# Kernel optimization log

Hardware: AMD Instinct MI355X
Metric: run time of the kernel (lower is better)

The kernel has to match this reference:

```python
import jax, jax.numpy as jnp
import numpy as np

N = 50000
E = 1600000
F = 128
G = 64  # number of graphs in the batch


def gat_layer(x, src, dst, W, a_src, a_dst, bias, heads, out_dim, concat):
    n = x.shape[0]
    h = (x @ W).reshape(n, heads, out_dim)                      # [N,H,D]
    alpha_src = jnp.sum(h * a_src, axis=-1)                     # [N,H]
    alpha_dst = jnp.sum(h * a_dst, axis=-1)                     # [N,H]
    e = jax.nn.leaky_relu(alpha_src[src] + alpha_dst[dst], negative_slope=0.2)  # [E,H]
    # segment softmax over edges grouped by destination node
    m = jax.ops.segment_max(e, dst, num_segments=n)
    m = jnp.where(jnp.isfinite(m), m, 0.0)
    ex = jnp.exp(e - m[dst])
    denom = jax.ops.segment_sum(ex, dst, num_segments=n)
    alpha = ex / (denom[dst] + 1e-16)                           # [E,H]
    msg = h[src] * alpha[:, :, None]                            # [E,H,D]
    out = jax.ops.segment_sum(msg, dst, num_segments=n)         # [N,H,D]
    if concat:
        out = out.reshape(n, heads * out_dim)
    else:
        out = out.mean(axis=1)
    return out + bias


def setup_inputs() -> dict:
    key = jax.random.key(0)
    ks = jax.random.split(key, 12)
    x = jax.random.normal(ks[0], (N, F), dtype=jnp.float32)
    edge_index = jax.random.randint(ks[1], (2, E), 0, N, dtype=jnp.int32)
    batch = jnp.sort(jax.random.randint(ks[2], (N,), 0, G, dtype=jnp.int32))
    s = 0.1
    W1 = jax.random.normal(ks[3], (F, 4 * 32), dtype=jnp.float32) * s
    a_src1 = jax.random.normal(ks[4], (4, 32), dtype=jnp.float32) * s
    a_dst1 = jax.random.normal(ks[5], (4, 32), dtype=jnp.float32) * s
    b1 = jnp.zeros((4 * 32,), dtype=jnp.float32)
    W2 = jax.random.normal(ks[6], (4 * 32, 2 * 16), dtype=jnp.float32) * s
    a_src2 = jax.random.normal(ks[7], (2, 16), dtype=jnp.float32) * s
    a_dst2 = jax.random.normal(ks[8], (2, 16), dtype=jnp.float32) * s
    b2 = jnp.zeros((16,), dtype=jnp.float32)
    fcW = jax.random.normal(ks[9], (16, 1), dtype=jnp.float32) * s
    fcb = jnp.zeros((1,), dtype=jnp.float32)
    return {"x": x, "edge_index": edge_index, "batch": batch,
            "W1": W1, "a_src1": a_src1, "a_dst1": a_dst1, "b1": b1,
            "W2": W2, "a_src2": a_src2, "a_dst2": a_dst2, "b2": b2,
            "fcW": fcW, "fcb": fcb}


def reference(x, edge_index, batch, W1, a_src1, a_dst1, b1, W2, a_src2, a_dst2, b2, fcW, fcb):
    n = x.shape[0]
    # PyG GATConv default: add self loops
    loops = jnp.arange(n, dtype=edge_index.dtype)
    src = jnp.concatenate([edge_index[0], loops])
    dst = jnp.concatenate([edge_index[1], loops])
    # eval mode: dropouts are no-ops
    h = jax.nn.relu(gat_layer(x, src, dst, W1, a_src1, a_dst1, b1, 4, 32, True))
    h = gat_layer(h, src, dst, W2, a_src2, a_dst2, b2, 2, 16, False)
    # global mean pool over graphs
    sums = jax.ops.segment_sum(h, batch, num_segments=G)        # [G,16]
    counts = jax.ops.segment_sum(jnp.ones((n,), h.dtype), batch, num_segments=G)
    pooled = sums / jnp.maximum(counts, 1.0)[:, None]
    return pooled @ fcW + fcb                                   # [G,1]
```

## Files before the change

kernel.cpp:

```cpp
#include <hip/hip_runtime.h>

#define LRELU(x) ((x) > 0.f ? (x) : 0.2f*(x))
typedef unsigned int uint;

__device__ inline unsigned short f2bf(float f) {
    union { float f; unsigned u; } v; v.f = f;
    unsigned r = v.u + 0x7FFF + ((v.u >> 16) & 1);
    return (unsigned short)(r >> 16);
}
__device__ inline uint packbf(float a, float b) {
    return (uint)f2bf(a) | ((uint)f2bf(b) << 16);
}
__device__ inline float bflo(uint u){ union{uint u; float f;}v; v.u = u<<16; return v.f; }
__device__ inline float bfhi(uint u){ union{uint u; float f;}v; v.u = u & 0xFFFF0000u; return v.f; }
__device__ inline float f4get(const float4& v, int i) {
    return i==0 ? v.x : i==1 ? v.y : i==2 ? v.z : v.w;
}


#define CSR_SHIFT 7
#define CSR_NBLK  512

__global__ __launch_bounds__(256) void bucket_count_kernel(
    const int* __restrict__ dst, int E, int chunk, int nb,
    int* __restrict__ blockCntT)
{
    __shared__ int cnt[1024];
    int t = threadIdx.x, k = blockIdx.x;
    for (int i = t; i < nb; i += 256) cnt[i] = 0;
    __syncthreads();
    int e0 = k * chunk, e1 = min(e0 + chunk, E);
    for (int e = e0 + t; e < e1; e += 256)
        atomicAdd(&cnt[dst[e] >> CSR_SHIFT], 1);
    __syncthreads();
    for (int b = t; b < nb; b += 256)
        blockCntT[b * CSR_NBLK + k] = cnt[b];
}

__global__ __launch_bounds__(512) void row_scan_kernel(
    int* __restrict__ blockCntT, int* __restrict__ tot)
{
    __shared__ int sm[512];
    int b = blockIdx.x, t = threadIdx.x;
    int* row = blockCntT + b * CSR_NBLK;
    int v = row[t];
    sm[t] = v;
    __syncthreads();
    for (int off = 1; off < 512; off <<= 1) {
        int u = (t >= off) ? sm[t - off] : 0;
        __syncthreads(); sm[t] += u; __syncthreads();
    }
    row[t] = sm[t] - v;
    if (t == 511) tot[b] = sm[511];
}

__global__ __launch_bounds__(1024) void total_scan_kernel(
    const int* __restrict__ tot, int nb, int* __restrict__ bucketBase)
{
    __shared__ int sm[1024];
    int t = threadIdx.x;
    int v = (t < nb) ? tot[t] : 0;
    sm[t] = v;
    __syncthreads();
    for (int off = 1; off < 1024; off <<= 1) {
        int u = (t >= off) ? sm[t - off] : 0;
        __syncthreads(); sm[t] += u; __syncthreads();
    }
    if (t < nb) bucketBase[t] = sm[t] - v;
    if (t == 1023) bucketBase[nb] = sm[1023];
}

__global__ __launch_bounds__(256) void bucket_scatter_kernel(
    const int* __restrict__ src, const int* __restrict__ dst, int E, int chunk, int nb,
    const int* __restrict__ blockCntT, const int* __restrict__ bucketBase,
    uint* __restrict__ ebuf)
{
    __shared__ int cur[1024];
    int t = threadIdx.x, k = blockIdx.x;
    for (int b = t; b < nb; b += 256)
        cur[b] = bucketBase[b] + blockCntT[b * CSR_NBLK + k];
    __syncthreads();
    int e0 = k * chunk, e1 = min(e0 + chunk, E);
    for (int e = e0 + t; e < e1; e += 256) {
        int d = dst[e], s_ = src[e];
        int pos = atomicAdd(&cur[d >> CSR_SHIFT], 1);
        ebuf[pos] = ((uint)s_ << 7) | (uint)(d & 127);
    }
}

__global__ __launch_bounds__(256) void local_csr_kernel(
    const uint* __restrict__ ebuf, const int* __restrict__ bucketBase,
    int n, int E, int* __restrict__ rowptr, int* __restrict__ csr)
{
    __shared__ int lbase[1 << CSR_SHIFT];
    __shared__ int lcur[1 << CSR_SHIFT];
    __shared__ int ldeg[1 << CSR_SHIFT];
    int b = blockIdx.x, t = threadIdx.x;
    int n0 = b << CSR_SHIFT;
    int base = bucketBase[b], end = bucketBase[b + 1];
    if (t < (1 << CSR_SHIFT)) ldeg[t] = 0;
    __syncthreads();
    for (int e = base + t; e < end; e += 256)
        atomicAdd(&ldeg[ebuf[e] & 127], 1);
    __syncthreads();
    if (t == 0) {
        int run = base;
        for (int i = 0; i < (1 << CSR_SHIFT); ++i) {
            lbase[i] = run; lcur[i] = run; run += ldeg[i];
        }
    }
    __syncthreads();
    int node = n0 + t;
    if (t < (1 << CSR_SHIFT) && node < n) rowptr[node] = lbase[t];
    if (b == 0 && t == 0) rowptr[n] = E;
    for (int e = base + t; e < end; e += 256) {
        uint ed = ebuf[e];
        int pos = atomicAdd(&lcur[ed & 127], 1);
        csr[pos] = (int)(ed >> 7);
    }
}


template<int COLS, int HEADS>
__global__ __launch_bounds__(256) void gemm_alpha_kernel(
    const float* __restrict__ x, const float* __restrict__ W,
    const float* __restrict__ a_src, const float* __restrict__ a_dst,
    uint* __restrict__ hq, float* __restrict__ as_out,
    float* __restrict__ ad_out, int n)
{
    constexpr int K = 128;
    constexpr int CPT = COLS / 8;
    constexpr int NPT = 4;
    constexpr int DIM = COLS / HEADS;
    constexpr int TPH = DIM / CPT;
    constexpr int NSLOT = COLS / 4;
    __shared__ float4 WL[K * NSLOT];

    int t = threadIdx.x;
    for (int idx = t * 4; idx < K * COLS; idx += 1024) {
        float4 w = *(const float4*)(W + idx);
        int k = idx / COLS, c = idx % COLS;
        int slot = c >> 2;
        if (COLS == 128) slot = (slot >> 2) | ((slot & 3) << 3);
        WL[k * NSLOT + slot] = w;
    }
    __syncthreads();

    int m_ = t & 7;
    int node0 = blockIdx.x * (32 * NPT) + (t >> 3) * NPT;
    if (node0 >= n) return;
    int c0 = m_ * CPT;

    const float* xr[NPT];
#pragma unroll
    for (int i = 0; i < NPT; i++) xr[i] = x + (size_t)min(node0 + i, n - 1) * K;

    float acc[NPT][CPT];
#pragma unroll
    for (int i = 0; i < NPT; i++)
#pragma unroll
        for (int q = 0; q < CPT; q++) acc[i][q] = 0.f;

    for (int k4 = 0; k4 < K; k4 += 4) {
        float4 xv[NPT];
#pragma unroll
        for (int i = 0; i < NPT; i++) xv[i] = *(const float4*)(xr[i] + k4);
#pragma unroll
        for (int kk = 0; kk < 4; kk++) {
#pragma unroll
            for (int j = 0; j < CPT / 4; j++) {
                int slot = (COLS == 128) ? (m_ | (j << 3)) : m_;
                float4 w = WL[(k4 + kk) * NSLOT + slot];
#pragma unroll
                for (int i = 0; i < NPT; i++) {
                    float xa = f4get(xv[i], kk);
                    acc[i][j*4+0] += xa * w.x;
                    acc[i][j*4+1] += xa * w.y;
                    acc[i][j*4+2] += xa * w.z;
                    acc[i][j*4+3] += xa * w.w;
                }
            }
        }
    }

    int head = c0 / DIM, lc = c0 - head * DIM;
    float asc[CPT], adc[CPT];
#pragma unroll
    for (int q = 0; q < CPT; q++) {
        asc[q] = a_src[head * DIM + lc + q];
        adc[q] = a_dst[head * DIM + lc + q];
    }

#pragma unroll
    for (int i = 0; i < NPT; i++) {
        int node = node0 + i;
        if (node >= n) break;
        if constexpr (COLS == 128) {
            uint wds[4];
#pragma unroll
            for (int j = 0; j < 4; j++) {
                int u = 0;
                u = __builtin_amdgcn_cvt_pk_fp8_f32(acc[i][j*4+0], acc[i][j*4+1], u, false);
                u = __builtin_amdgcn_cvt_pk_fp8_f32(acc[i][j*4+2], acc[i][j*4+3], u, true);
                wds[j] = (uint)u;
            }
            *(uint4*)(hq + (size_t)node * 32 + m_ * 4) = make_uint4(wds[0], wds[1], wds[2], wds[3]);
        } else {
            uint w0 = packbf(acc[i][0], acc[i][1]);
            uint w1 = packbf(acc[i][2], acc[i][3]);
            *(uint2*)(hq + (size_t)node * 16 + m_ * 2) = make_uint2(w0, w1);
        }
        float ps = 0.f, pd = 0.f;
#pragma unroll
        for (int q = 0; q < CPT; q++) {
            ps += acc[i][q] * asc[q];
            pd += acc[i][q] * adc[q];
        }
#pragma unroll
        for (int off = 1; off < TPH; off <<= 1) {
            ps += __shfl_xor(ps, off);
            pd += __shfl_xor(pd, off);
        }
        if ((m_ & (TPH - 1)) == 0) {
            as_out[node * HEADS + head] = ps;
            ad_out[node * HEADS + head] = pd;
        }
    }
}


__global__ __launch_bounds__(256) void agg1_kernel(
    const float* __restrict__ as1f, const float* __restrict__ ad1f,
    const uint* __restrict__ h1q, const int* __restrict__ rowptr,
    const int* __restrict__ csr, const float* __restrict__ b1,
    float* __restrict__ hout, int n)
{
    int t = threadIdx.x;
    int w = t >> 6, tw = t & 63;
    int g = tw >> 3, l = tw & 7;
    int head = l >> 1;
    int node = blockIdx.x * 4 + w;
    if (node >= n) return;

    float adh = ad1f[node * 4 + head];
    int rp = rowptr[node], re = rowptr[node + 1];

    float acc[16];
#pragma unroll
    for (int i = 0; i < 16; i++) acc[i] = 0.f;
    float den = 0.f;

#pragma unroll 2
    for (int e = rp + g; e < re; e += 8) {
        int s = csr[e];
        float a = as1f[s * 4 + head];
        uint4 u = *(const uint4*)(h1q + ((size_t)s << 5) + (l << 2));
        float ex = __expf(LRELU(a + adh));
        den += ex;
        uint ua[4] = {u.x, u.y, u.z, u.w};
#pragma unroll
        for (int j = 0; j < 4; j++) {
            auto p0 = __builtin_amdgcn_cvt_pk_f32_fp8(ua[j], false);
            auto p1 = __builtin_amdgcn_cvt_pk_f32_fp8(ua[j], true);
            acc[j*4+0] += ex * p0[0]; acc[j*4+1] += ex * p0[1];
            acc[j*4+2] += ex * p1[0]; acc[j*4+3] += ex * p1[1];
        }
    }

    if (g == 0) {
        float a = as1f[node * 4 + head];
        float ex = __expf(LRELU(a + adh));
        den += ex;
        uint4 u = *(const uint4*)(h1q + ((size_t)node << 5) + (l << 2));
        uint ua[4] = {u.x, u.y, u.z, u.w};
#pragma unroll
        for (int j = 0; j < 4; j++) {
            auto p0 = __builtin_amdgcn_cvt_pk_f32_fp8(ua[j], false);
            auto p1 = __builtin_amdgcn_cvt_pk_f32_fp8(ua[j], true);
            acc[j*4+0] += ex * p0[0]; acc[j*4+1] += ex * p0[1];
            acc[j*4+2] += ex * p1[0]; acc[j*4+3] += ex * p1[1];
        }
    }

#pragma unroll
    for (int i = 0; i < 16; i++) {
        acc[i] += __shfl_xor(acc[i], 8);
        acc[i] += __shfl_xor(acc[i], 16);
        acc[i] += __shfl_xor(acc[i], 32);
    }
    den += __shfl_xor(den, 8);
    den += __shfl_xor(den, 16);
    den += __shfl_xor(den, 32);

    if (g == 0) {
        float inv = 1.f / (den + 1e-16f);
        const float4* b4 = (const float4*)b1;
#pragma unroll
        for (int j = 0; j < 4; j++) {
            float4 bv = b4[(l << 2) + j];
            float4 o;
            o.x = fmaxf(acc[j*4+0] * inv + bv.x, 0.f);
            o.y = fmaxf(acc[j*4+1] * inv + bv.y, 0.f);
            o.z = fmaxf(acc[j*4+2] * inv + bv.z, 0.f);
            o.w = fmaxf(acc[j*4+3] * inv + bv.w, 0.f);
            ((float4*)hout)[(size_t)node * 32 + (l << 2) + j] = o;
        }
    }
}


__global__ __launch_bounds__(256) void agg2_kernel(
    const float* __restrict__ as2f, const float* __restrict__ ad2f,
    const uint* __restrict__ h2q, const int* __restrict__ rowptr,
    const int* __restrict__ csr, const float* __restrict__ b2,
    float* __restrict__ hf, int n)
{
    int t = threadIdx.x;
    int w = t >> 6, tw = t & 63;
    int g = tw >> 3, l = tw & 7;
    int head = l >> 2;
    int node = blockIdx.x * 4 + w;
    if (node >= n) return;

    float adh = ad2f[node * 2 + head];
    int rp = rowptr[node], re = rowptr[node + 1];

    float acc[4] = {0.f, 0.f, 0.f, 0.f};
    float den = 0.f;

#pragma unroll 2
    for (int e = rp + g; e < re; e += 8) {
        int s = csr[e];
        float a = as2f[s * 2 + head];
        uint2 u = *(const uint2*)(h2q + ((size_t)s << 4) + (l << 1));
        float ex = __expf(LRELU(a + adh));
        den += ex;
        acc[0] += ex * bflo(u.x); acc[1] += ex * bfhi(u.x);
        acc[2] += ex * bflo(u.y); acc[3] += ex * bfhi(u.y);
    }

    if (g == 0) {
        float a = as2f[node * 2 + head];
        float ex = __expf(LRELU(a + adh));
        den += ex;
        uint2 u = *(const uint2*)(h2q + ((size_t)node << 4) + (l << 1));
        acc[0] += ex * bflo(u.x); acc[1] += ex * bfhi(u.x);
        acc[2] += ex * bflo(u.y); acc[3] += ex * bfhi(u.y);
    }

#pragma unroll
    for (int i = 0; i < 4; i++) {
        acc[i] += __shfl_xor(acc[i], 8);
        acc[i] += __shfl_xor(acc[i], 16);
        acc[i] += __shfl_xor(acc[i], 32);
    }
    den += __shfl_xor(den, 8);
    den += __shfl_xor(den, 16);
    den += __shfl_xor(den, 32);

    float inv = 1.f / (den + 1e-16f);
    float v0 = acc[0] * inv, v1 = acc[1] * inv, v2 = acc[2] * inv, v3 = acc[3] * inv;
    float o0 = 0.5f * (v0 + __shfl_xor(v0, 4));
    float o1 = 0.5f * (v1 + __shfl_xor(v1, 4));
    float o2 = 0.5f * (v2 + __shfl_xor(v2, 4));
    float o3 = 0.5f * (v3 + __shfl_xor(v3, 4));
    if (g == 0 && l < 4) {
        float4 o;
        o.x = o0 + b2[4*l+0]; o.y = o1 + b2[4*l+1];
        o.z = o2 + b2[4*l+2]; o.w = o3 + b2[4*l+3];
        *(float4*)(hf + (size_t)node * 16 + 4 * l) = o;
    }
}


__global__ __launch_bounds__(256) void pool_kernel(
    const float* __restrict__ hf, const int* __restrict__ batch,
    float* __restrict__ sums, float* __restrict__ counts, int n)
{
    int t = threadIdx.x;
    int d = t & 15, j = t >> 4;
    int base = blockIdx.x * 256 + j * 16;
    float run = 0.f, cnt = 0.f;
    int cg = -1;
    for (int i = 0; i < 16; ++i) {
        int nn = base + i;
        if (nn >= n) break;
        int g = batch[nn];
        if (g != cg) {
            if (cg >= 0) { atomicAdd(&sums[cg * 16 + d], run); if (d == 0) atomicAdd(&counts[cg], cnt); }
            cg = g; run = 0.f; cnt = 0.f;
        }
        run += hf[(size_t)nn * 16 + d];
        cnt += 1.f;
    }
    if (cg >= 0) { atomicAdd(&sums[cg * 16 + d], run); if (d == 0) atomicAdd(&counts[cg], cnt); }
}

__global__ void final_kernel(const float* __restrict__ sums, const float* __restrict__ counts,
                             const float* __restrict__ fcW, const float* __restrict__ fcb,
                             float* __restrict__ out, int G)
{
    int g = blockIdx.x * 64 + threadIdx.x;
    if (g < G) {
        float c = fmaxf(counts[g], 1.f);
        float s = 0.f;
        for (int dd = 0; dd < 16; ++dd) s += (sums[g * 16 + dd] / c) * fcW[dd];
        out[g] = s + fcb[0];
    }
}


extern "C" void kernel_launch(void* const* d_in, const int* in_sizes, int n_in,
                              void* d_out, int out_size, void* d_ws, size_t ws_size,
                              hipStream_t stream)
{
    const float* x      = (const float*)d_in[0];
    const int*   ei     = (const int*)d_in[1];
    const int*   batch  = (const int*)d_in[2];
    const float* W1     = (const float*)d_in[3];
    const float* a_src1 = (const float*)d_in[4];
    const float* a_dst1 = (const float*)d_in[5];
    const float* b1     = (const float*)d_in[6];
    const float* W2     = (const float*)d_in[7];
    const float* a_src2 = (const float*)d_in[8];
    const float* a_dst2 = (const float*)d_in[9];
    const float* b2     = (const float*)d_in[10];
    const float* fcW    = (const float*)d_in[11];
    const float* fcb    = (const float*)d_in[12];
    float* out = (float*)d_out;

    int n = in_sizes[0] / 128;
    int E = in_sizes[1] / 2;
    int G = out_size;
    const int* srcA = ei;
    const int* dstA = ei + E;

    int nb = (n + (1 << CSR_SHIFT) - 1) >> CSR_SHIFT;
    int chunk = (E + CSR_NBLK - 1) / CSR_NBLK;

    char* p = (char*)d_ws;
    auto alloc = [&](size_t bytes) { char* r = p; p += (bytes + 255) & ~(size_t)255; return r; };
    int*   blockCntT  = (int*)alloc((size_t)nb * CSR_NBLK * 4);
    int*   tot        = (int*)alloc((size_t)nb * 4);
    int*   bucketBase = (int*)alloc((size_t)(nb + 1) * 4);
    int*   rowptr     = (int*)alloc((size_t)(n + 1) * 4);
    int*   csr        = (int*)alloc((size_t)E * 4);
    uint*  h1q        = (uint*)alloc((size_t)n * 32 * 4);
    float* as1        = (float*)alloc((size_t)n * 16);
    float* ad1        = (float*)alloc((size_t)n * 16);
    float* hrelu      = (float*)alloc((size_t)n * 128 * 4);
    uint*  h2q        = (uint*)alloc((size_t)n * 16 * 4);
    float* as2        = (float*)alloc((size_t)n * 8);
    float* ad2        = (float*)alloc((size_t)n * 8);
    float* hf         = (float*)alloc((size_t)n * 16 * 4);
    float* sums       = (float*)alloc((size_t)G * 16 * 4 + (size_t)G * 4);
    float* counts     = sums + G * 16;

    uint* ebuf = (uint*)hrelu;

    hipMemsetAsync(sums, 0, (size_t)G * 16 * 4 + (size_t)G * 4, stream);

    bucket_count_kernel<<<CSR_NBLK, 256, 0, stream>>>(dstA, E, chunk, nb, blockCntT);
    row_scan_kernel<<<nb, 512, 0, stream>>>(blockCntT, tot);
    total_scan_kernel<<<1, 1024, 0, stream>>>(tot, nb, bucketBase);
    bucket_scatter_kernel<<<CSR_NBLK, 256, 0, stream>>>(srcA, dstA, E, chunk, nb,
                                                        blockCntT, bucketBase, ebuf);
    local_csr_kernel<<<nb, 256, 0, stream>>>(ebuf, bucketBase, n, E, rowptr, csr);

    int gb = (n + 127) / 128;
    gemm_alpha_kernel<128, 4><<<gb, 256, 0, stream>>>(x, W1, a_src1, a_dst1, h1q, as1, ad1, n);
    agg1_kernel<<<(n + 3) / 4, 256, 0, stream>>>(as1, ad1, h1q, rowptr, csr, b1, hrelu, n);
    gemm_alpha_kernel<32, 2><<<gb, 256, 0, stream>>>(hrelu, W2, a_src2, a_dst2, h2q, as2, ad2, n);
    agg2_kernel<<<(n + 3) / 4, 256, 0, stream>>>(as2, ad2, h2q, rowptr, csr, b2, hf, n);
    pool_kernel<<<(n + 255) / 256, 256, 0, stream>>>(hf, batch, sums, counts, n);
    final_kernel<<<1, 64, 0, stream>>>(sums, counts, fcW, fcb, out, G);
}
```

Before: 195.9 us.

## Store layer-1 output in bf16, fuse total scan, use nontemporal CSR loads

The layer-1 aggregation now writes its ReLU output as packed bf16, and the second GEMM reads it in bf16. This halves the intermediate write and read traffic. The separate total-scan kernel is folded into row_scan, where the last block, found through an atomic counter, performs the bucket scan, removing one launch. CSR index loads in both aggregation kernels use nontemporal hints. The bf16 intermediate lowers precision of layer-2 inputs, and the last-block pattern relies on threadfence ordering plus a zeroed counter.

```diff
diff --git a/kernel.cpp b/kernel.cpp
--- a/kernel.cpp
+++ b/kernel.cpp
@@ -2,20 +2,18 @@
 
 #define LRELU(x) ((x) > 0.f ? (x) : 0.2f*(x))
 typedef unsigned int uint;
-
-__device__ inline unsigned short f2bf(float f) {
+typedef unsigned short ushort;
+
+__device__ inline ushort f2bf(float f) {
     union { float f; unsigned u; } v; v.f = f;
     unsigned r = v.u + 0x7FFF + ((v.u >> 16) & 1);
-    return (unsigned short)(r >> 16);
+    return (ushort)(r >> 16);
 }
 __device__ inline uint packbf(float a, float b) {
     return (uint)f2bf(a) | ((uint)f2bf(b) << 16);
 }
 __device__ inline float bflo(uint u){ union{uint u; float f;}v; v.u = u<<16; return v.f; }
 __device__ inline float bfhi(uint u){ union{uint u; float f;}v; v.u = u & 0xFFFF0000u; return v.f; }
-__device__ inline float f4get(const float4& v, int i) {
-    return i==0 ? v.x : i==1 ? v.y : i==2 ? v.z : v.w;
-}
 
 
 #define CSR_SHIFT 7
@@ -38,9 +36,11 @@
 }
 
 __global__ __launch_bounds__(512) void row_scan_kernel(
-    int* __restrict__ blockCntT, int* __restrict__ tot)
+    int* __restrict__ blockCntT, int* __restrict__ tot,
+    int* __restrict__ bucketBase, int nb, int* __restrict__ done)
 {
     __shared__ int sm[512];
+    __shared__ int isLast;
     int b = blockIdx.x, t = threadIdx.x;
     int* row = blockCntT + b * CSR_NBLK;
     int v = row[t];
@@ -52,22 +52,21 @@
     }
     row[t] = sm[t] - v;
     if (t == 511) tot[b] = sm[511];
-}
-
-__global__ __launch_bounds__(1024) void total_scan_kernel(
-    const int* __restrict__ tot, int nb, int* __restrict__ bucketBase)
-{
-    __shared__ int sm[1024];
-    int t = threadIdx.x;
-    int v = (t < nb) ? tot[t] : 0;
-    sm[t] = v;
-    __syncthreads();
-    for (int off = 1; off < 1024; off <<= 1) {
-        int u = (t >= off) ? sm[t - off] : 0;
-        __syncthreads(); sm[t] += u; __syncthreads();
-    }
-    if (t < nb) bucketBase[t] = sm[t] - v;
-    if (t == 1023) bucketBase[nb] = sm[1023];
+    __threadfence();
+    if (t == 0) isLast = (atomicAdd(done, 1) == gridDim.x - 1);
+    __syncthreads();
+    if (isLast) {
+        __threadfence();
+        int w = (t < nb) ? tot[t] : 0;
+        sm[t] = w;
+        __syncthreads();
+        for (int off = 1; off < 512; off <<= 1) {
+            int u = (t >= off) ? sm[t - off] : 0;
+            __syncthreads(); sm[t] += u; __syncthreads();
+        }
+        if (t < nb) bucketBase[t] = sm[t] - w;
+        if (t == 511) bucketBase[nb] = sm[511];
+    }
 }
 
 __global__ __launch_bounds__(256) void bucket_scatter_kernel(
@@ -121,9 +120,9 @@
 }
 
 
-template<int COLS, int HEADS>
+template<int COLS, int HEADS, bool XBF16>
 __global__ __launch_bounds__(256) void gemm_alpha_kernel(
-    const float* __restrict__ x, const float* __restrict__ W,
+    const void* __restrict__ xin, const float* __restrict__ W,
     const float* __restrict__ a_src, const float* __restrict__ a_dst,
     uint* __restrict__ hq, float* __restrict__ as_out,
     float* __restrict__ ad_out, int n)
@@ -151,9 +150,9 @@
     if (node0 >= n) return;
     int c0 = m_ * CPT;
 
-    const float* xr[NPT];
-#pragma unroll
-    for (int i = 0; i < NPT; i++) xr[i] = x + (size_t)min(node0 + i, n - 1) * K;
+    size_t rows[NPT];
+#pragma unroll
+    for (int i = 0; i < NPT; i++) rows[i] = (size_t)min(node0 + i, n - 1);
 
     float acc[NPT][CPT];
 #pragma unroll
@@ -162,9 +161,18 @@
         for (int q = 0; q < CPT; q++) acc[i][q] = 0.f;
 
     for (int k4 = 0; k4 < K; k4 += 4) {
-        float4 xv[NPT];
-#pragma unroll
-        for (int i = 0; i < NPT; i++) xv[i] = *(const float4*)(xr[i] + k4);
+        float xs[NPT][4];
+#pragma unroll
+        for (int i = 0; i < NPT; i++) {
+            if constexpr (XBF16) {
+                uint2 u = *(const uint2*)((const uint*)xin + rows[i] * 64 + (k4 >> 1));
+                xs[i][0] = bflo(u.x); xs[i][1] = bfhi(u.x);
+                xs[i][2] = bflo(u.y); xs[i][3] = bfhi(u.y);
+            } else {
+                float4 v = *(const float4*)((const float*)xin + rows[i] * 128 + k4);
+                xs[i][0] = v.x; xs[i][1] = v.y; xs[i][2] = v.z; xs[i][3] = v.w;
+            }
+        }
 #pragma unroll
         for (int kk = 0; kk < 4; kk++) {
 #pragma unroll
@@ -173,7 +181,7 @@
                 float4 w = WL[(k4 + kk) * NSLOT + slot];
 #pragma unroll
                 for (int i = 0; i < NPT; i++) {
-                    float xa = f4get(xv[i], kk);
+                    float xa = xs[i][kk];
                     acc[i][j*4+0] += xa * w.x;
                     acc[i][j*4+1] += xa * w.y;
                     acc[i][j*4+2] += xa * w.z;
@@ -233,7 +241,7 @@
     const float* __restrict__ as1f, const float* __restrict__ ad1f,
     const uint* __restrict__ h1q, const int* __restrict__ rowptr,
     const int* __restrict__ csr, const float* __restrict__ b1,
-    float* __restrict__ hout, int n)
+    uint* __restrict__ hrelu, int n)
 {
     int t = threadIdx.x;
     int w = t >> 6, tw = t & 63;
@@ -252,7 +260,7 @@
 
 #pragma unroll 2
     for (int e = rp + g; e < re; e += 8) {
-        int s = csr[e];
+        int s = __builtin_nontemporal_load(csr + e);
         float a = as1f[s * 4 + head];
         uint4 u = *(const uint4*)(h1q + ((size_t)s << 5) + (l << 2));
         float ex = __expf(LRELU(a + adh));
@@ -294,17 +302,19 @@
 
     if (g == 0) {
         float inv = 1.f / (den + 1e-16f);
-        const float4* b4 = (const float4*)b1;
+        uint o[8];
 #pragma unroll
         for (int j = 0; j < 4; j++) {
-            float4 bv = b4[(l << 2) + j];
-            float4 o;
-            o.x = fmaxf(acc[j*4+0] * inv + bv.x, 0.f);
-            o.y = fmaxf(acc[j*4+1] * inv + bv.y, 0.f);
-            o.z = fmaxf(acc[j*4+2] * inv + bv.z, 0.f);
-            o.w = fmaxf(acc[j*4+3] * inv + bv.w, 0.f);
-            ((float4*)hout)[(size_t)node * 32 + (l << 2) + j] = o;
-        }
+            float v0 = fmaxf(acc[j*4+0] * inv + b1[16*l + 4*j + 0], 0.f);
+            float v1 = fmaxf(acc[j*4+1] * inv + b1[16*l + 4*j + 1], 0.f);
+            float v2 = fmaxf(acc[j*4+2] * inv + b1[16*l + 4*j + 2], 0.f);
+            float v3 = fmaxf(acc[j*4+3] * inv + b1[16*l + 4*j + 3], 0.f);
+            o[2*j]   = packbf(v0, v1);
+            o[2*j+1] = packbf(v2, v3);
+        }
+        uint* hp = hrelu + (size_t)node * 64 + l * 8;
+        *(uint4*)hp       = make_uint4(o[0], o[1], o[2], o[3]);
+        *(uint4*)(hp + 4) = make_uint4(o[4], o[5], o[6], o[7]);
     }
 }
 
@@ -330,7 +340,7 @@
 
 #pragma unroll 2
     for (int e = rp + g; e < re; e += 8) {
-        int s = csr[e];
+        int s = __builtin_nontemporal_load(csr + e);
         float a = as2f[s * 2 + head];
         uint2 u = *(const uint2*)(h2q + ((size_t)s << 4) + (l << 1));
         float ex = __expf(LRELU(a + adh));
@@ -448,29 +458,31 @@
     uint*  h1q        = (uint*)alloc((size_t)n * 32 * 4);
     float* as1        = (float*)alloc((size_t)n * 16);
     float* ad1        = (float*)alloc((size_t)n * 16);
-    float* hrelu      = (float*)alloc((size_t)n * 128 * 4);
+    uint*  hrelu      = (uint*)alloc((size_t)n * 64 * 4);
     uint*  h2q        = (uint*)alloc((size_t)n * 16 * 4);
     float* as2        = (float*)alloc((size_t)n * 8);
     float* ad2        = (float*)alloc((size_t)n * 8);
     float* hf         = (float*)alloc((size_t)n * 16 * 4);
-    float* sums       = (float*)alloc((size_t)G * 16 * 4 + (size_t)G * 4);
+    float* sums       = (float*)alloc((size_t)(G * 16 + G + 1) * 4);
     float* counts     = sums + G * 16;
+    int*   done       = (int*)(counts + G);
 
     uint* ebuf = (uint*)hrelu;
 
-    hipMemsetAsync(sums, 0, (size_t)G * 16 * 4 + (size_t)G * 4, stream);
+    hipMemsetAsync(sums, 0, (size_t)(G * 16 + G + 1) * 4, stream);
 
     bucket_count_kernel<<<CSR_NBLK, 256, 0, stream>>>(dstA, E, chunk, nb, blockCntT);
-    row_scan_kernel<<<nb, 512, 0, stream>>>(blockCntT, tot);
-    total_scan_kernel<<<1, 1024, 0, stream>>>(tot, nb, bucketBase);
+    row_scan_kernel<<<nb, 512, 0, stream>>>(blockCntT, tot, bucketBase, nb, done);
     bucket_scatter_kernel<<<CSR_NBLK, 256, 0, stream>>>(srcA, dstA, E, chunk, nb,
                                                         blockCntT, bucketBase, ebuf);
     local_csr_kernel<<<nb, 256, 0, stream>>>(ebuf, bucketBase, n, E, rowptr, csr);
 
     int gb = (n + 127) / 128;
-    gemm_alpha_kernel<128, 4><<<gb, 256, 0, stream>>>(x, W1, a_src1, a_dst1, h1q, as1, ad1, n);
+    gemm_alpha_kernel<128, 4, false><<<gb, 256, 0, stream>>>(x, W1, a_src1, a_dst1,
+                                                             h1q, as1, ad1, n);
     agg1_kernel<<<(n + 3) / 4, 256, 0, stream>>>(as1, ad1, h1q, rowptr, csr, b1, hrelu, n);
-    gemm_alpha_kernel<32, 2><<<gb, 256, 0, stream>>>(hrelu, W2, a_src2, a_dst2, h2q, as2, ad2, n);
+    gemm_alpha_kernel<32, 2, true><<<gb, 256, 0, stream>>>(hrelu, W2, a_src2, a_dst2,
+                                                           h2q, as2, ad2, n);
     agg2_kernel<<<(n + 3) / 4, 256, 0, stream>>>(as2, ad2, h2q, rowptr, csr, b2, hf, n);
     pool_kernel<<<(n + 255) / 256, 256, 0, stream>>>(hf, batch, sums, counts, n);
     final_kernel<<<1, 64, 0, stream>>>(sums, counts, fcW, fcb, out, G);
```

After: 254.9 us. 1.3x slower.
